# Performance work log

Measured on AMD Instinct MI355X. Metric: run time of the kernel, lower is better.

Reference implementation:

```python
import jax, jax.numpy as jnp
import numpy as np

N = 50000       # nodes
E = 800000      # edges
IN = 256        # input channels
H = 4           # heads
C = 64          # hidden channels per head
NEG_SLOPE = 0.2 # PyG GATConv default LeakyReLU slope
EPS = 1e-16


def setup_inputs() -> dict:
    key = jax.random.key(0)
    k_x, k_e, k_w, k_as, k_ad = jax.random.split(key, 5)
    x = jax.random.normal(k_x, (N, IN), dtype=jnp.float32)
    edge_index = jax.random.randint(k_e, (2, E), 0, N, dtype=jnp.int64)
    # GATConv params: glorot-style scale
    W = jax.random.normal(k_w, (IN, H * C), dtype=jnp.float32) * (1.0 / np.sqrt(IN))
    att_src = jax.random.normal(k_as, (H, C), dtype=jnp.float32) * (1.0 / np.sqrt(C))
    att_dst = jax.random.normal(k_ad, (H, C), dtype=jnp.float32) * (1.0 / np.sqrt(C))
    return {"x": x, "edge_index": edge_index, "W": W, "att_src": att_src, "att_dst": att_dst}


def reference(x, edge_index, W, att_src, att_dst):
    src, dst = edge_index[0], edge_index[1]
    # linear projection, split heads: [N, H, C]
    xh = (x @ W).reshape(N, H, C)
    # per-node attention halves: [N, H]
    a_src = jnp.einsum('nhc,hc->nh', xh, att_src)
    a_dst = jnp.einsum('nhc,hc->nh', xh, att_dst)
    # per-edge logits with LeakyReLU: [E, H]
    alpha = a_src[src] + a_dst[dst]
    alpha = jnp.where(alpha >= 0, alpha, NEG_SLOPE * alpha)
    # segment softmax over destination nodes
    m = jax.ops.segment_max(alpha, dst, num_segments=N)          # [N, H]
    ex = jnp.exp(alpha - m[dst])                                  # [E, H]
    denom = jax.ops.segment_sum(ex, dst, num_segments=N)         # [N, H]
    att = ex / (denom[dst] + EPS)                                 # [E, H]
    # weighted message scatter-add: [N, H, C] -> concat heads [N, H*C]
    msg = att[:, :, None] * xh[src]                               # [E, H, C]
    out = jax.ops.segment_sum(msg, dst, num_segments=N)
    out = out.reshape(N, H * C)
    return (out, att)
```

## Files before the change

### kernel.cpp

```cpp
#include <hip/hip_runtime.h>
#include <math.h>

#define IN_CH   256
#define HC      256
#define H_HEADS 4
#define NEG_SLOPE 0.2f
#define LOG2E   1.44269504088896f
#define DEFER_THR 12.0f
#define MINIT   -3.0e38f

typedef __attribute__((ext_vector_type(8))) short short8;
typedef __attribute__((ext_vector_type(4))) short short4v;
typedef __attribute__((ext_vector_type(4))) float float4v;

__device__ __forceinline__ float bf2f(unsigned short b) {
    return __uint_as_float(((unsigned)b) << 16);
}
__device__ __forceinline__ unsigned short f2bf(float f) {
    unsigned u = __float_as_uint(f);
    u += 0x7fffu + ((u >> 16) & 1u);
    return (unsigned short)(u >> 16);
}
__device__ __forceinline__ float lrelu(float a) {
    return a >= 0.f ? a : NEG_SLOPE * a;
}
__device__ __forceinline__ float fexp2(float a) {
    return __builtin_amdgcn_exp2f(a);
}


__global__ void prep_w(const float* __restrict__ w,
                       unsigned short* __restrict__ wt) {
    int idx = blockIdx.x * 256 + threadIdx.x;
    int k = idx >> 8, c = idx & 255;
    wt[(size_t)c * 256 + k] = f2bf(w[idx]);
}

__global__ __launch_bounds__(256) void gemm_xh(const float* __restrict__ x,
                                               const unsigned short* __restrict__ wt,
                                               const float* __restrict__ att_s,
                                               const float* __restrict__ att_d,
                                               unsigned short* __restrict__ xh_bf,
                                               float* __restrict__ a_src,
                                               float* __restrict__ a_dst, int N) {
    __shared__ __attribute__((aligned(16))) unsigned char lds_a[16384];
    int tid  = threadIdx.x;
    int wave = tid >> 6;
    int lane = tid & 63;
    int quad = lane >> 4;
    int l16  = lane & 15;
    int rb   = blockIdx.x * 16;

#pragma unroll
    for (int pass = 0; pass < 2; ++pass) {
        int s  = pass * 256 + tid;
        int kc = s >> 4;
        int m  = s & 15;
        int grow = rb + m; if (grow >= N) grow = N - 1;
        const float* gp = x + (size_t)grow * IN_CH + kc * 8;
        float4v f0 = *(const float4v*)gp;
        float4v f1 = *(const float4v*)(gp + 4);
        short8 hi, lo;
#pragma unroll
        for (int j = 0; j < 4; ++j) {
            unsigned short h0 = f2bf(f0[j]);
            hi[j] = (short)h0;
            lo[j] = (short)f2bf(f0[j] - bf2f(h0));
            unsigned short h1 = f2bf(f1[j]);
            hi[4 + j] = (short)h1;
            lo[4 + j] = (short)f2bf(f1[j] - bf2f(h1));
        }
        *(short8*)(lds_a + (size_t)s * 16) = hi;
        *(short8*)(lds_a + 8192 + (size_t)s * 16) = lo;
    }
    __syncthreads();

    float4v acc[4] = {};
    const unsigned short* wt_base = wt + ((size_t)wave * 64 + l16) * IN_CH;
#pragma unroll
    for (int k0 = 0; k0 < 8; ++k0) {
        int kc   = k0 * 4 + quad;
        int slot = kc * 16 + l16;
        short8 a_hi = *(const short8*)(lds_a + slot * 16);
        short8 a_lo = *(const short8*)(lds_a + 8192 + slot * 16);
#pragma unroll
        for (int ct = 0; ct < 4; ++ct) {
            short8 bh = *(const short8*)(wt_base + (size_t)ct * 16 * IN_CH
                                         + k0 * 32 + quad * 8);
            acc[ct] = __builtin_amdgcn_mfma_f32_16x16x32_bf16(a_lo, bh, acc[ct], 0, 0, 0);
            acc[ct] = __builtin_amdgcn_mfma_f32_16x16x32_bf16(a_hi, bh, acc[ct], 0, 0, 0);
        }
    }

    int cb = wave;
    float ps[4] = {0.f, 0.f, 0.f, 0.f};
    float pd[4] = {0.f, 0.f, 0.f, 0.f};
#pragma unroll
    for (int ct = 0; ct < 4; ++ct) {
        float as_c = att_s[cb * 64 + ct * 16 + l16] * LOG2E;
        float ad_c = att_d[cb * 64 + ct * 16 + l16] * LOG2E;
#pragma unroll
        for (int r = 0; r < 4; ++r) {
            float v = acc[ct][r];
            int grow = rb + quad * 4 + r;
            if (grow < N)
                xh_bf[(size_t)grow * HC + cb * 64 + ct * 16 + l16] = f2bf(v);
            ps[r] += v * as_c;
            pd[r] += v * ad_c;
        }
    }
#pragma unroll
    for (int off = 1; off < 16; off <<= 1) {
#pragma unroll
        for (int r = 0; r < 4; ++r) {
            ps[r] += __shfl_xor(ps[r], off);
            pd[r] += __shfl_xor(pd[r], off);
        }
    }
    if (l16 == 0) {
#pragma unroll
        for (int r = 0; r < 4; ++r) {
            int grow = rb + quad * 4 + r;
            if (grow < N) {
                a_src[(size_t)grow * 4 + cb] = ps[r];
                a_dst[(size_t)grow * 4 + cb] = pd[r];
            }
        }
    }
}

__global__ __launch_bounds__(256) void deg_count(const int* __restrict__ ei,
                                                 int* __restrict__ deg, int E) {
    int e = blockIdx.x * 256 + threadIdx.x;
    if (e >= E) return;
    atomicAdd(deg + ei[E + e], 1);
}


__global__ __launch_bounds__(256) void scan_part(const int* __restrict__ deg,
                                                 int* __restrict__ part, int N) {
    int t = threadIdx.x;
    int base = blockIdx.x * 1024 + t * 4;
    int s = 0;
    if (base + 4 <= N) {
        int4 v = *(const int4*)(deg + base);
        s = v.x + v.y + v.z + v.w;
    } else {
#pragma unroll
        for (int j = 0; j < 4; ++j)
            if (base + j < N) s += deg[base + j];
    }
#pragma unroll
    for (int off = 1; off < 64; off <<= 1) s += __shfl_xor(s, off);
    __shared__ int ws[4];
    if ((t & 63) == 0) ws[t >> 6] = s;
    __syncthreads();
    if (t == 0) part[blockIdx.x] = ws[0] + ws[1] + ws[2] + ws[3];
}

__global__ __launch_bounds__(256) void scan_final(const int* __restrict__ deg,
                                                  const int* __restrict__ part,
                                                  int* __restrict__ rowptr,
                                                  int* __restrict__ cursor, int N) {
    __shared__ int sm[256];
    __shared__ int wsum[4];
    int t = threadIdx.x;
    int bacc = 0;
    for (int j = t; j < blockIdx.x; j += 256) bacc += part[j];
#pragma unroll
    for (int off = 1; off < 64; off <<= 1) bacc += __shfl_xor(bacc, off);
    if ((t & 63) == 0) wsum[t >> 6] = bacc;

    int base = blockIdx.x * 1024 + t * 4;
    int v0 = 0, v1 = 0, v2 = 0, v3 = 0;
    if (base + 4 <= N) {
        int4 v = *(const int4*)(deg + base);
        v0 = v.x; v1 = v.y; v2 = v.z; v3 = v.w;
    } else {
        if (base + 0 < N) v0 = deg[base + 0];
        if (base + 1 < N) v1 = deg[base + 1];
        if (base + 2 < N) v2 = deg[base + 2];
        if (base + 3 < N) v3 = deg[base + 3];
    }
    int s = v0 + v1 + v2 + v3;
    sm[t] = s;
    __syncthreads();
    for (int off = 1; off < 256; off <<= 1) {
        int tmp = (t >= off) ? sm[t - off] : 0;
        __syncthreads();
        sm[t] += tmp;
        __syncthreads();
    }
    int boff = wsum[0] + wsum[1] + wsum[2] + wsum[3];
    int run = boff + sm[t] - s;
    int r0 = run, r1 = r0 + v0, r2 = r1 + v1, r3 = r2 + v2;
    if (base + 4 <= N) {
        *(int4*)(rowptr + base) = (int4){r0, r1, r2, r3};
        *(int4*)(cursor + base) = (int4){r0, r1, r2, r3};
    } else {
        if (base + 0 < N) { rowptr[base + 0] = r0; cursor[base + 0] = r0; }
        if (base + 1 < N) { rowptr[base + 1] = r1; cursor[base + 1] = r1; }
        if (base + 2 < N) { rowptr[base + 2] = r2; cursor[base + 2] = r2; }
        if (base + 3 < N) { rowptr[base + 3] = r3; cursor[base + 3] = r3; }
    }
}

__global__ __launch_bounds__(256) void fill_csr(const int* __restrict__ ei,
                                                const float* __restrict__ a_src,
                                                const float* __restrict__ a_dst,
                                                int* __restrict__ cursor,
                                                int* __restrict__ csr_off,
                                                float* __restrict__ csr_al,
                                                float* __restrict__ al_e, int E) {
    int e = blockIdx.x * 256 + threadIdx.x;
    if (e >= E) return;
    int s = ei[e], d = ei[E + e];
    float4v as = *(const float4v*)(a_src + (size_t)s * 4);
    float4v ad = *(const float4v*)(a_dst + (size_t)d * 4);
    float4v al;
#pragma unroll
    for (int h = 0; h < 4; ++h) al[h] = lrelu(as[h] + ad[h]);
    int slot = atomicAdd(cursor + d, 1);
    csr_off[slot] = s << 9;
    *(float4v*)(csr_al + (size_t)slot * 4) = al;
    *(float4v*)(al_e + (size_t)e * 4) = al;
}

__global__ __launch_bounds__(256) void gat_gather(const int* __restrict__ csr_off,
                                                  const float* __restrict__ csr_al,
                                                  const int* __restrict__ rowptr,
                                                  const int* __restrict__ deg,
                                                  const unsigned short* __restrict__ xh_bf,
                                                  float* __restrict__ out,
                                                  float* __restrict__ pack, int N) {
    int wave = threadIdx.x >> 6, lane = threadIdx.x & 63;
    int half = lane >> 5;
    int l32  = lane & 31;
    int h    = l32 >> 3;
    int d    = blockIdx.x * 8 + wave * 2 + half;
    bool dv  = d < N;
    int dc   = dv ? d : N - 1;
    int start = rowptr[dc];
    int cnt   = dv ? deg[dc] : 0;
    int cntMax = max(cnt, __shfl_xor(cnt, 32));

    const char* xb = (const char*)xh_bf;
    int lboff = l32 * 16;

    float mE = MINIT, lE = 0.f, mO = MINIT, lO = 0.f;
    float accE[8] = {0.f, 0.f, 0.f, 0.f, 0.f, 0.f, 0.f, 0.f};
    float accO[8] = {0.f, 0.f, 0.f, 0.f, 0.f, 0.f, 0.f, 0.f};

#define LOFF(idx) (((idx) < cnt) ? csr_off[start + (idx)] : 0)
#define LAL(idx)  (((idx) < cnt) ? csr_al[(size_t)(start + (idx)) * 4 + h] : -INFINITY)

    int oE = LOFF(0), oO = LOFF(1);
    float alE = LAL(0), alO = LAL(1);
    short8 xvE = *(const short8*)(xb + (size_t)oE + lboff);
    short8 xvO = *(const short8*)(xb + (size_t)oO + lboff);
    int oE2 = LOFF(2), oO2 = LOFF(3);

    for (int i = 0; i < cntMax; i += 2) {
        float alE_n = LAL(i + 2), alO_n = LAL(i + 3);
        short8 xvE_n = *(const short8*)(xb + (size_t)oE2 + lboff);
        short8 xvO_n = *(const short8*)(xb + (size_t)oO2 + lboff);
        int oE3 = LOFF(i + 4), oO3 = LOFF(i + 5);

        bool ok = (alE <= mE + DEFER_THR) && (alO <= mO + DEFER_THR);
        if (__all(ok)) {
            float p = fexp2(alE - mE);
            float q = fexp2(alO - mO);
            lE += p; lO += q;
#pragma unroll
            for (int j = 0; j < 8; ++j) {
                accE[j] += p * bf2f((unsigned short)xvE[j]);
                accO[j] += q * bf2f((unsigned short)xvO[j]);
            }
        } else {
            float mnE = fmaxf(mE, alE);
            float scE = fexp2(mE - mnE);
            float pE  = fexp2(alE - mnE);
            lE = lE * scE + pE;
            float mnO = fmaxf(mO, alO);
            float scO = fexp2(mO - mnO);
            float pO  = fexp2(alO - mnO);
            lO = lO * scO + pO;
#pragma unroll
            for (int j = 0; j < 8; ++j) {
                accE[j] = accE[j] * scE + pE * bf2f((unsigned short)xvE[j]);
                accO[j] = accO[j] * scO + pO * bf2f((unsigned short)xvO[j]);
            }
            mE = mnE; mO = mnO;
        }
        alE = alE_n; alO = alO_n; xvE = xvE_n; xvO = xvO_n;
        oE2 = oE3; oO2 = oO3;
    }
#undef LOFF
#undef LAL

    float mm = fmaxf(mE, mO);
    float sE = fexp2(mE - mm), sO = fexp2(mO - mm);
    float l  = lE * sE + lO * sO;
    float inv = 1.f / (l + 1e-16f);
    if (dv) {
        float4v o0, o1;
#pragma unroll
        for (int j = 0; j < 4; ++j) {
            o0[j] = (accE[j] * sE + accO[j] * sO) * inv;
            o1[j] = (accE[4 + j] * sE + accO[4 + j] * sO) * inv;
        }
        float* orow = out + (size_t)d * HC + l32 * 8;
        *(float4v*)orow = o0;
        *(float4v*)(orow + 4) = o1;
        if ((l32 & 7) == 0) {
            pack[(size_t)d * 8 + h]     = mm;
            pack[(size_t)d * 8 + 4 + h] = inv;
        }
    }
}

__global__ __launch_bounds__(256) void att_edge(const int* __restrict__ ei,
                                                const float* __restrict__ al_e,
                                                const float* __restrict__ pack,
                                                float* __restrict__ att_out, int E) {
    int e = blockIdx.x * 256 + threadIdx.x;
    if (e >= E) return;
    int d = ei[E + e];
    float4v al = *(const float4v*)(al_e + (size_t)e * 4);
    float4v mm = *(const float4v*)(pack + (size_t)d * 8);
    float4v gg = *(const float4v*)(pack + (size_t)d * 8 + 4);
    float4v o;
#pragma unroll
    for (int h = 0; h < 4; ++h)
        o[h] = fexp2(al[h] - mm[h]) * gg[h];
    *(float4v*)(att_out + (size_t)e * 4) = o;
}

extern "C" void kernel_launch(void* const* d_in, const int* in_sizes, int n_in,
                              void* d_out, int out_size, void* d_ws, size_t ws_size,
                              hipStream_t stream) {
    const float* x     = (const float*)d_in[0];
    const int*   ei    = (const int*)d_in[1];
    const float* W     = (const float*)d_in[2];
    const float* att_s = (const float*)d_in[3];
    const float* att_d = (const float*)d_in[4];

    const int N = in_sizes[0] / IN_CH;
    const int E = in_sizes[1] / 2;

    char* ws = (char*)d_ws;
    size_t off = 0;
    unsigned short* xh_bf = (unsigned short*)(ws + off); off += (size_t)N * HC * 2;
    unsigned short* wt    = (unsigned short*)(ws + off); off += (size_t)IN_CH * HC * 2;
    float* a_src = (float*)(ws + off); off += (size_t)N * H_HEADS * 4;
    float* a_dst = (float*)(ws + off); off += (size_t)N * H_HEADS * 4;
    float* pack  = (float*)(ws + off); off += (size_t)N * 8 * 4;
    int* rowptr  = (int*)(ws + off); off += (size_t)N * 4;
    int* cursor  = (int*)(ws + off); off += (size_t)N * 4;
    int* csr_off = (int*)(ws + off); off += (size_t)E * 4;
    float* csr_al = (float*)(ws + off); off += (size_t)E * 4 * 4;
    float* al_e   = (float*)(ws + off); off += (size_t)E * 4 * 4;
    int* part    = (int*)(ws + off); off += 1024 * 4;
    size_t zoff = off;
    int* deg     = (int*)(ws + off); off += (size_t)N * 4;

    float* out     = (float*)d_out;
    float* out_att = out + (size_t)N * HC;

    (void)hipMemsetAsync(ws + zoff, 0, off - zoff, stream);

    const int NB = (N + 1023) / 1024;

    prep_w<<<256, 256, 0, stream>>>(W, wt);
    deg_count<<<(E + 255) / 256, 256, 0, stream>>>(ei, deg, E);
    gemm_xh<<<(N + 15) / 16, 256, 0, stream>>>(x, wt, att_s, att_d,
                                               xh_bf, a_src, a_dst, N);
    scan_part<<<NB, 256, 0, stream>>>(deg, part, N);
    scan_final<<<NB, 256, 0, stream>>>(deg, part, rowptr, cursor, N);
    fill_csr<<<(E + 255) / 256, 256, 0, stream>>>(ei, a_src, a_dst, cursor,
                                                  csr_off, csr_al, al_e, E);
    gat_gather<<<(N + 7) / 8, 256, 0, stream>>>(csr_off, csr_al, rowptr, deg,
                                                xh_bf, out, pack, N);
    att_edge<<<(E + 255) / 256, 256, 0, stream>>>(ei, al_e, pack, out_att, E);
}
```

Baseline: 322.6 us.

## Recompute edge logits in att_edge and deepen gather prefetch pipeline

The per-edge logit buffer al_e (E×4 floats) is no longer written in fill_csr and read back in att_edge. att_edge instead gathers a_src and a_dst by node index and recomputes the LeakyReLU logit, trading a streaming read and write for two random node-indexed reads. The gather kernel now prefetches neighbour features two pairs ahead instead of one, and offset loads use a clamped index rather than a count check, so out-of-range lanes read valid real rows that carry -inf logits. This hides more gather latency at the cost of extra registers.

```diff
diff --git a/kernel.cpp b/kernel.cpp
--- a/kernel.cpp
+++ b/kernel.cpp
@@ -210,8 +210,7 @@
                                                 const float* __restrict__ a_dst,
                                                 int* __restrict__ cursor,
                                                 int* __restrict__ csr_off,
-                                                float* __restrict__ csr_al,
-                                                float* __restrict__ al_e, int E) {
+                                                float* __restrict__ csr_al, int E) {
     int e = blockIdx.x * 256 + threadIdx.x;
     if (e >= E) return;
     int s = ei[e], d = ei[E + e];
@@ -223,7 +222,6 @@
     int slot = atomicAdd(cursor + d, 1);
     csr_off[slot] = s << 9;
     *(float4v*)(csr_al + (size_t)slot * 4) = al;
-    *(float4v*)(al_e + (size_t)e * 4) = al;
 }
 
 __global__ __launch_bounds__(256) void gat_gather(const int* __restrict__ csr_off,
@@ -232,7 +230,8 @@
                                                   const int* __restrict__ deg,
                                                   const unsigned short* __restrict__ xh_bf,
                                                   float* __restrict__ out,
-                                                  float* __restrict__ pack, int N) {
+                                                  float* __restrict__ pack,
+                                                  int N, int E) {
     int wave = threadIdx.x >> 6, lane = threadIdx.x & 63;
     int half = lane >> 5;
     int l32  = lane & 31;
@@ -243,6 +242,7 @@
     int start = rowptr[dc];
     int cnt   = dv ? deg[dc] : 0;
     int cntMax = max(cnt, __shfl_xor(cnt, 32));
+    int emax = E - 1;
 
     const char* xb = (const char*)xh_bf;
     int lboff = l32 * 16;
@@ -251,20 +251,23 @@
     float accE[8] = {0.f, 0.f, 0.f, 0.f, 0.f, 0.f, 0.f, 0.f};
     float accO[8] = {0.f, 0.f, 0.f, 0.f, 0.f, 0.f, 0.f, 0.f};
 
-#define LOFF(idx) (((idx) < cnt) ? csr_off[start + (idx)] : 0)
+#define LOFF(idx) (csr_off[min(start + (idx), emax)])
 #define LAL(idx)  (((idx) < cnt) ? csr_al[(size_t)(start + (idx)) * 4 + h] : -INFINITY)
 
-    int oE = LOFF(0), oO = LOFF(1);
-    float alE = LAL(0), alO = LAL(1);
-    short8 xvE = *(const short8*)(xb + (size_t)oE + lboff);
-    short8 xvO = *(const short8*)(xb + (size_t)oO + lboff);
-    int oE2 = LOFF(2), oO2 = LOFF(3);
-
+    int o4 = LOFF(4), o5 = LOFF(5);
+    float alE  = LAL(0), alO  = LAL(1);
+    float alE1 = LAL(2), alO1 = LAL(3);
+    short8 xvE  = *(const short8*)(xb + (size_t)(unsigned)LOFF(0) + lboff);
+    short8 xvO  = *(const short8*)(xb + (size_t)(unsigned)LOFF(1) + lboff);
+    short8 xvE1 = *(const short8*)(xb + (size_t)(unsigned)LOFF(2) + lboff);
+    short8 xvO1 = *(const short8*)(xb + (size_t)(unsigned)LOFF(3) + lboff);
+
+#pragma unroll 2
     for (int i = 0; i < cntMax; i += 2) {
-        float alE_n = LAL(i + 2), alO_n = LAL(i + 3);
-        short8 xvE_n = *(const short8*)(xb + (size_t)oE2 + lboff);
-        short8 xvO_n = *(const short8*)(xb + (size_t)oO2 + lboff);
-        int oE3 = LOFF(i + 4), oO3 = LOFF(i + 5);
+        short8 xvE2 = *(const short8*)(xb + (size_t)(unsigned)o4 + lboff);
+        short8 xvO2 = *(const short8*)(xb + (size_t)(unsigned)o5 + lboff);
+        int o6 = LOFF(i + 6), o7 = LOFF(i + 7);
+        float alE2 = LAL(i + 4), alO2 = LAL(i + 5);
 
         bool ok = (alE <= mE + DEFER_THR) && (alO <= mO + DEFER_THR);
         if (__all(ok)) {
@@ -292,8 +295,9 @@
             }
             mE = mnE; mO = mnO;
         }
-        alE = alE_n; alO = alO_n; xvE = xvE_n; xvO = xvO_n;
-        oE2 = oE3; oO2 = oO3;
+        alE = alE1; alO = alO1; alE1 = alE2; alO1 = alO2;
+        xvE = xvE1; xvO = xvO1; xvE1 = xvE2; xvO1 = xvO2;
+        o4 = o6; o5 = o7;
     }
 #undef LOFF
 #undef LAL
@@ -320,19 +324,21 @@
 }
 
 __global__ __launch_bounds__(256) void att_edge(const int* __restrict__ ei,
-                                                const float* __restrict__ al_e,
+                                                const float* __restrict__ a_src,
+                                                const float* __restrict__ a_dst,
                                                 const float* __restrict__ pack,
                                                 float* __restrict__ att_out, int E) {
     int e = blockIdx.x * 256 + threadIdx.x;
     if (e >= E) return;
-    int d = ei[E + e];
-    float4v al = *(const float4v*)(al_e + (size_t)e * 4);
+    int s = ei[e], d = ei[E + e];
+    float4v as = *(const float4v*)(a_src + (size_t)s * 4);
+    float4v ad = *(const float4v*)(a_dst + (size_t)d * 4);
     float4v mm = *(const float4v*)(pack + (size_t)d * 8);
     float4v gg = *(const float4v*)(pack + (size_t)d * 8 + 4);
     float4v o;
 #pragma unroll
     for (int h = 0; h < 4; ++h)
-        o[h] = fexp2(al[h] - mm[h]) * gg[h];
+        o[h] = fexp2(lrelu(as[h] + ad[h]) - mm[h]) * gg[h];
     *(float4v*)(att_out + (size_t)e * 4) = o;
 }
 
@@ -358,8 +364,7 @@
     int* rowptr  = (int*)(ws + off); off += (size_t)N * 4;
     int* cursor  = (int*)(ws + off); off += (size_t)N * 4;
     int* csr_off = (int*)(ws + off); off += (size_t)E * 4;
-    float* csr_al = (float*)(ws + off); off += (size_t)E * 4 * 4;
-    float* al_e   = (float*)(ws + off); off += (size_t)E * 4 * 4;
+    float* csr_al = (float*)(ws + off); off += (size_t)E * 4 * 4 + 256;
     int* part    = (int*)(ws + off); off += 1024 * 4;
     size_t zoff = off;
     int* deg     = (int*)(ws + off); off += (size_t)N * 4;
@@ -378,8 +383,9 @@
     scan_part<<<NB, 256, 0, stream>>>(deg, part, N);
     scan_final<<<NB, 256, 0, stream>>>(deg, part, rowptr, cursor, N);
     fill_csr<<<(E + 255) / 256, 256, 0, stream>>>(ei, a_src, a_dst, cursor,
-                                                  csr_off, csr_al, al_e, E);
+                                                  csr_off, csr_al, E);
     gat_gather<<<(N + 7) / 8, 256, 0, stream>>>(csr_off, csr_al, rowptr, deg,
-                                                xh_bf, out, pack, N);
-    att_edge<<<(E + 255) / 256, 256, 0, stream>>>(ei, al_e, pack, out_att, E);
-}
+                                                xh_bf, out, pack, N, E);
+    att_edge<<<(E + 255) / 256, 256, 0, stream>>>(ei, a_src, a_dst, pack,
+                                                  out_att, E);
+}
```

After: 339.2 us. +5.1%, slower.
